# Performance work log

Hardware: AMD Instinct MI355X
Metric: run time of the kernel (lower is better)

The kernel has to match this reference:

```python
import jax, jax.numpy as jnp
import numpy as np

H = 32        # query heads
KV = 8        # key/value heads
D = 128       # head_dim
GROUPS = H // KV
THETA = 10000.0


def _rope_cos_sin(position_ids):
    # position_ids: [B, S] int
    inv_freq = 1.0 / (THETA ** (jnp.arange(0, D, 2, dtype=jnp.float32) / D))  # [D/2]
    freqs = position_ids.astype(jnp.float32)[:, :, None] * inv_freq[None, None, :]  # [B,S,D/2]
    emb = jnp.concatenate([freqs, freqs], axis=-1)  # [B,S,D]
    return jnp.cos(emb), jnp.sin(emb)


def _rotate_half(x):
    x1, x2 = jnp.split(x, 2, axis=-1)
    return jnp.concatenate([-x2, x1], axis=-1)


def _apply_rope(x, cos, sin):
    # x: [B,h,S,D]; cos/sin: [B,S,D] -> broadcast over heads
    return x * cos[:, None, :, :] + _rotate_half(x) * sin[:, None, :, :]


def setup_inputs() -> dict:
    key = jax.random.key(0)
    ks = jax.random.split(key, 8)
    B, S, Dm = 2, 2048, 4096
    scale = lambda d: 1.0 / np.sqrt(d)
    hidden_states = jax.random.normal(ks[0], (B, S, Dm), dtype=jnp.float32)
    position_ids = jnp.broadcast_to(jnp.arange(S, dtype=jnp.int32)[None, :], (B, S))
    Wq = jax.random.normal(ks[1], (Dm, H * D), dtype=jnp.float32) * scale(Dm)
    Wk = jax.random.normal(ks[2], (Dm, KV * D), dtype=jnp.float32) * scale(Dm)
    Wv = jax.random.normal(ks[3], (Dm, KV * D), dtype=jnp.float32) * scale(Dm)
    Wo = jax.random.normal(ks[4], (H * D, Dm), dtype=jnp.float32) * scale(H * D)
    # per-head shift-encoder correction weights (small init so it's a correction)
    Ws_q = jax.random.normal(ks[5], (H, D, D), dtype=jnp.float32) * (0.02 * scale(D))
    Ws_k = jax.random.normal(ks[6], (H, D, D), dtype=jnp.float32) * (0.02 * scale(D))
    return {"hidden_states": hidden_states, "position_ids": position_ids,
            "Wq": Wq, "Wk": Wk, "Wv": Wv, "Wo": Wo, "Ws_q": Ws_q, "Ws_k": Ws_k}


def reference(hidden_states, position_ids, Wq, Wk, Wv, Wo, Ws_q, Ws_k):
    B, S, Dm = hidden_states.shape
    # projections -> [B, heads, S, D]
    q = (hidden_states @ Wq).reshape(B, S, H, D).transpose(0, 2, 1, 3)
    k = (hidden_states @ Wk).reshape(B, S, KV, D).transpose(0, 2, 1, 3)
    v = (hidden_states @ Wv).reshape(B, S, KV, D).transpose(0, 2, 1, 3)
    # RoPE
    cos, sin = _rope_cos_sin(position_ids)
    q = _apply_rope(q, cos, sin)
    k = _apply_rope(k, cos, sin)
    # GQA repeat_kv: [B,KV,S,D] -> [B,H,S,D]
    k = jnp.repeat(k, GROUPS, axis=1)
    v = jnp.repeat(v, GROUPS, axis=1)
    # causal SDPA
    scores = jnp.einsum('bhqd,bhkd->bhqk', q, k) / jnp.sqrt(jnp.float32(D))
    causal = jnp.tril(jnp.ones((S, S), dtype=bool))
    scores = jnp.where(causal[None, None, :, :], scores, jnp.float32(-1e30))
    probs = jax.nn.softmax(scores, axis=-1)
    attn = jnp.einsum('bhqk,bhkd->bhqd', probs, v)  # [B,H,S,D]
    attn = attn.transpose(0, 2, 1, 3)               # [B,S,H,D]
    # shift_encoder.do_shift: per-head linear correction from rotated Q and K
    delta = jnp.einsum('bhsd,hde->bshe', q, Ws_q) + jnp.einsum('bhsd,hde->bshe', k, Ws_k)
    attn = attn + delta
    # output projection
    out = attn.reshape(B, S, H * D) @ Wo
    return out
```

## Files before the change

### kernel.cpp

```cpp
#include <hip/hip_runtime.h>
#include <cstdint>

#define DEV __device__ __forceinline__

typedef __attribute__((ext_vector_type(4))) float  f32x4;
typedef __attribute__((ext_vector_type(8))) short  s16x8;
typedef __attribute__((ext_vector_type(4))) unsigned short u16x4;
typedef __attribute__((ext_vector_type(8))) unsigned short u16x8;

constexpr int B_   = 2;
constexpr int S_   = 2048;
constexpr int DM   = 4096;
constexpr int HQ   = 32;
constexpr int KVH  = 8;
constexpr int DH   = 128;
constexpr int NQKV = 6144;

DEV unsigned short f2bf(float f) {
  union { float f; unsigned u; } c; c.f = f;
  unsigned u = c.u + 0x7FFFu + ((c.u >> 16) & 1u);
  return (unsigned short)(u >> 16);
}
DEV float bf2f(unsigned short h) {
  union { unsigned u; float f; } c; c.u = (unsigned)h << 16; return c.f;
}
DEV void gload16(const void* g, const void* l) {
  __builtin_amdgcn_global_load_lds(
      (const __attribute__((address_space(1))) unsigned int*)(uintptr_t)g,
      (__attribute__((address_space(3))) unsigned int*)(unsigned)(uintptr_t)l,
      16, 0, 0);
}
DEV f32x4 mfma16x16(s16x8 a, s16x8 b, f32x4 c) {
  return __builtin_amdgcn_mfma_f32_16x16x32_bf16(a, b, c, 0, 0, 0);
}

__global__ __launch_bounds__(256) void k_tables(const int* __restrict__ pos,
                                                float* __restrict__ ct,
                                                float* __restrict__ st) {
  int i = blockIdx.x * 256 + threadIdx.x;
  if (i >= B_ * S_ * 64) return;
  int f = i & 63, bs = i >> 6;
  float p   = (float)pos[bs];
  float inv = __builtin_amdgcn_exp2f(-(float)f * 0.20762050593048355f);
  float a   = p * inv;
  ct[i] = cosf(a);
  st[i] = sinf(a);
}

__global__ __launch_bounds__(256) void k_cvt(const float* __restrict__ in,
                                             unsigned short* __restrict__ out,
                                             int n8) {
  int i = blockIdx.x * 256 + threadIdx.x;
  if (i >= n8) return;
  const f32x4* p = (const f32x4*)in + (size_t)2 * i;
  f32x4 a = p[0], b = p[1];
  u16x8 o;
  o[0] = f2bf(a[0]); o[1] = f2bf(a[1]); o[2] = f2bf(a[2]); o[3] = f2bf(a[3]);
  o[4] = f2bf(b[0]); o[5] = f2bf(b[1]); o[6] = f2bf(b[2]); o[7] = f2bf(b[3]);
  ((u16x8*)out)[i] = o;
}

__global__ __launch_bounds__(256) void k_tconv(const float* __restrict__ in,
                                               unsigned short* __restrict__ out,
                                               int R, int C,
                                               unsigned long long ibs,
                                               unsigned long long obs) {
  __shared__ float t[64][65];
  const int r0 = blockIdx.y * 64, c0 = blockIdx.x * 64;
  const float* ib = in + (size_t)blockIdx.z * ibs;
  unsigned short* ob = out + (size_t)blockIdx.z * obs;
  const int tid = threadIdx.x, tr = tid >> 4, c4 = (tid & 15) * 4;
#pragma unroll
  for (int it = 0; it < 4; ++it) {
    int rr = it * 16 + tr;
    f32x4 v = *(const f32x4*)&ib[(size_t)(r0 + rr) * C + (c0 + c4)];
    t[rr][c4 + 0] = v[0]; t[rr][c4 + 1] = v[1];
    t[rr][c4 + 2] = v[2]; t[rr][c4 + 3] = v[3];
  }
  __syncthreads();
#pragma unroll
  for (int it = 0; it < 4; ++it) {
    int cc = it * 16 + tr;
    u16x4 o;
    o[0] = f2bf(t[c4 + 0][cc]); o[1] = f2bf(t[c4 + 1][cc]);
    o[2] = f2bf(t[c4 + 2][cc]); o[3] = f2bf(t[c4 + 3][cc]);
    *(u16x4*)&ob[(size_t)(c0 + cc) * R + (r0 + c4)] = o;
  }
}

template <int BF16OUT>
__global__ __launch_bounds__(512, 2) void k_gemm256(const unsigned short* __restrict__ A,
                                                    const unsigned short* __restrict__ BT,
                                                    void* __restrict__ Cv,
                                                    int M, int N, int K, int NBX) {
  extern __shared__ __align__(16) char L[];
  const int tid = threadIdx.x;
  const int lane = tid & 63, w = tid >> 6;
  const int g = lane >> 4, ml = lane & 15;
  const int wr = w & 1, wc = w >> 1;

  const int cpx = (int)gridDim.x >> 3;
  const int swz = ((int)blockIdx.x & 7) * cpx + ((int)blockIdx.x >> 3);
  const int by = swz / NBX, bx = swz - by * NBX;
  const int bm = by * 256, bn = bx * 256;

  const int srow_l = tid >> 3;
  const int scol_e = (((tid & 7) ^ ((tid >> 3) & 7)) << 3);
  const int nk = K >> 6;

#define STAGE(kt, hf) do {                                                        \
    if ((kt) < nk) {                                                              \
      const unsigned short* sb; char* db;                                         \
      if ((hf) < 2) { sb = A  + (size_t)(bm + (hf) * 128) * K;                    \
                      db = L + ((kt) & 1) * 32768 + (hf) * 16384; }               \
      else          { sb = BT + (size_t)(bn + ((hf) - 2) * 128) * K;              \
                      db = L + 65536 + ((kt) & 1) * 32768 + ((hf) - 2) * 16384; } \
      sb += (size_t)(kt) * 64 + scol_e;                                           \
      _Pragma("unroll")                                                           \
      for (int r_ = 0; r_ < 2; ++r_)                                              \
        gload16(sb + (size_t)(r_ * 64 + srow_l) * K, db + r_ * 8192 + w * 1024);  \
    } } while (0)

  f32x4 Z = {0.f, 0.f, 0.f, 0.f};
  f32x4 acc[8][4];
#pragma unroll
  for (int i = 0; i < 8; ++i)
#pragma unroll
    for (int j = 0; j < 4; ++j) acc[i][j] = Z;
  s16x8 bfr[4][2], afr[2][2];

#define FRAG(base, row, ks)                                                       \
  ((const s16x8*)((base) + ((((row) >> 7) * 16384 + ((row) & 127) * 128 +         \
                             ((ks) * 32 + 8 * g) * 2) ^ (((row) & 7) << 4))))

#define PHASE(q, kbuf, SKT, SHF, VM) do {                                         \
    if ((q) == 0) {                                                               \
      _Pragma("unroll")                                                           \
      for (int nf = 0; nf < 4; ++nf)                                              \
        _Pragma("unroll")                                                         \
        for (int ks = 0; ks < 2; ++ks)                                            \
          bfr[nf][ks] = *FRAG(L + 65536 + (kbuf) * 32768,                         \
                              wc * 64 + nf * 16 + ml, ks);                        \
    }                                                                             \
    _Pragma("unroll")                                                             \
    for (int mm = 0; mm < 2; ++mm)                                                \
      _Pragma("unroll")                                                           \
      for (int ks = 0; ks < 2; ++ks)                                              \
        afr[mm][ks] = *FRAG(L + (kbuf) * 32768,                                   \
                            32 * (2 * (q) + mm) + 16 * wr + ml, ks);              \
    STAGE(SKT, SHF);                                                              \
    if ((VM) == 1) { asm volatile("s_waitcnt vmcnt(6)" ::: "memory"); }           \
    else if ((VM) == 2) {                                                         \
      if (last) { asm volatile("s_waitcnt vmcnt(0)" ::: "memory"); }              \
      else      { asm volatile("s_waitcnt vmcnt(6)" ::: "memory"); }              \
    } else if ((VM) == 3) {                                                       \
      if (!last) { asm volatile("s_waitcnt vmcnt(6)" ::: "memory"); }             \
    }                                                                             \
    __builtin_amdgcn_s_barrier();                                                 \
    asm volatile("s_waitcnt lgkmcnt(0)" ::: "memory");                            \
    __builtin_amdgcn_sched_barrier(0);                                            \
    __builtin_amdgcn_s_setprio(1);                                                \
    _Pragma("unroll")                                                             \
    for (int mm = 0; mm < 2; ++mm)                                                \
      _Pragma("unroll")                                                           \
      for (int nf = 0; nf < 4; ++nf)                                              \
        _Pragma("unroll")                                                         \
        for (int ks = 0; ks < 2; ++ks)                                            \
          acc[2 * (q) + mm][nf] =                                                 \
              mfma16x16(afr[mm][ks], bfr[nf][ks], acc[2 * (q) + mm][nf]);         \
    __builtin_amdgcn_s_setprio(0);                                                \
    __builtin_amdgcn_s_barrier();                                                 \
  } while (0)

  STAGE(0, 0); STAGE(0, 1); STAGE(0, 2); STAGE(0, 3);
  STAGE(1, 2); STAGE(1, 3); STAGE(1, 0);
  asm volatile("s_waitcnt vmcnt(6)" ::: "memory");
  __builtin_amdgcn_s_barrier();

  const int iters = nk >> 1;
  for (int i = 0; i < iters; ++i) {
    const int k0 = 2 * i;
    const bool last = (i == iters - 1);
    PHASE(0, 0, k0 + 1, 1, 0);
    PHASE(1, 0, k0 + 2, 2, 0);
    PHASE(2, 0, k0 + 2, 0, 0);
    PHASE(3, 0, k0 + 2, 3, 2);
    PHASE(0, 1, k0 + 2, 1, 0);
    PHASE(1, 1, k0 + 3, 2, 0);
    PHASE(2, 1, k0 + 3, 3, 0);
    PHASE(3, 1, k0 + 3, 0, 3);
  }
#undef PHASE
#undef FRAG
#undef STAGE

  const int row0 = bm + 16 * wr + 4 * g, col0 = bn + wc * 64 + ml;
#pragma unroll
  for (int m = 0; m < 8; ++m)
#pragma unroll
    for (int nf = 0; nf < 4; ++nf)
#pragma unroll
      for (int r = 0; r < 4; ++r) {
        int row = row0 + 32 * m + r;
        int col = col0 + nf * 16;
        if (BF16OUT)
          ((unsigned short*)Cv)[(size_t)row * N + col] = f2bf(acc[m][nf][r]);
        else
          ((float*)Cv)[(size_t)row * N + col] = acc[m][nf][r];
      }
}

__global__ __launch_bounds__(256) void k_rope(const unsigned short* __restrict__ qkv,
                                              const float* __restrict__ ct,
                                              const float* __restrict__ st,
                                              unsigned short* __restrict__ qr,
                                              unsigned short* __restrict__ kr) {
  const int bs = blockIdx.x;
  const int b = bs >> 11, s = bs & 2047;
  const int tid = threadIdx.x;
  const float* cr = ct + (size_t)bs * 64;
  const float* sr = st + (size_t)bs * 64;
  const unsigned short* row = qkv + (size_t)bs * NQKV;
  {
    int h = tid >> 3, d0 = (tid & 7) * 16;
    u16x8 xs  = *(const u16x8*)&row[h * 128 + d0];
    u16x8 xs2 = *(const u16x8*)&row[h * 128 + d0 + 8];
    u16x8 xp  = *(const u16x8*)&row[h * 128 + (d0 ^ 64)];
    u16x8 xp2 = *(const u16x8*)&row[h * 128 + (d0 ^ 64) + 8];
    float sg = (d0 < 64) ? -1.f : 1.f;
    int ci = d0 & 63;
    u16x8 o1, o2;
#pragma unroll
    for (int j = 0; j < 8; ++j)
      o1[j] = f2bf(bf2f(xs[j]) * cr[ci + j] + sg * bf2f(xp[j]) * sr[ci + j]);
#pragma unroll
    for (int j = 0; j < 8; ++j)
      o2[j] = f2bf(bf2f(xs2[j]) * cr[ci + 8 + j] + sg * bf2f(xp2[j]) * sr[ci + 8 + j]);
    unsigned short* dst = qr + ((size_t)(b * HQ + h) * S_ + s) * DH + d0;
    *(u16x8*)dst = o1;
    *(u16x8*)(dst + 8) = o2;
  }
  if (tid < 64) {
    int kv = tid >> 3, d0 = (tid & 7) * 16;
    const unsigned short* krow = row + HQ * DH + kv * 128;
    u16x8 xs  = *(const u16x8*)&krow[d0];
    u16x8 xs2 = *(const u16x8*)&krow[d0 + 8];
    u16x8 xp  = *(const u16x8*)&krow[d0 ^ 64];
    u16x8 xp2 = *(const u16x8*)&krow[(d0 ^ 64) + 8];
    float sg = (d0 < 64) ? -1.f : 1.f;
    int ci = d0 & 63;
    u16x8 o1, o2;
#pragma unroll
    for (int j = 0; j < 8; ++j)
      o1[j] = f2bf(bf2f(xs[j]) * cr[ci + j] + sg * bf2f(xp[j]) * sr[ci + j]);
#pragma unroll
    for (int j = 0; j < 8; ++j)
      o2[j] = f2bf(bf2f(xs2[j]) * cr[ci + 8 + j] + sg * bf2f(xp2[j]) * sr[ci + 8 + j]);
    unsigned short* dst = kr + ((size_t)(b * KVH + kv) * S_ + s) * DH + d0;
    *(u16x8*)dst = o1;
    *(u16x8*)(dst + 8) = o2;
  }
}

__global__ __launch_bounds__(256) void k_vtrans(const unsigned short* __restrict__ qkv,
                                                unsigned short* __restrict__ vt) {
  __shared__ unsigned short t[64][65];
  const int z = blockIdx.z, b = z >> 3, kv = z & 7;
  const int s0 = blockIdx.x * 64, d0 = blockIdx.y * 64;
  const int tid = threadIdx.x, tr = tid >> 4, c4 = (tid & 15) * 4;
  const unsigned short* src = qkv + (size_t)(b * S_) * NQKV + HQ * DH + KVH * DH + kv * 128;
#pragma unroll
  for (int it = 0; it < 4; ++it) {
    int s = it * 16 + tr;
    u16x4 v = *(const u16x4*)&src[(size_t)(s0 + s) * NQKV + d0 + c4];
    t[s][c4 + 0] = v[0]; t[s][c4 + 1] = v[1];
    t[s][c4 + 2] = v[2]; t[s][c4 + 3] = v[3];
  }
  __syncthreads();
  unsigned short* dst = vt + (size_t)(b * KVH + kv) * DH * S_;
#pragma unroll
  for (int it = 0; it < 4; ++it) {
    int d = it * 16 + tr;
    u16x4 o;
    o[0] = t[c4 + 0][d]; o[1] = t[c4 + 1][d];
    o[2] = t[c4 + 2][d]; o[3] = t[c4 + 3][d];
    *(u16x4*)&dst[(size_t)(d0 + d) * S_ + s0 + c4] = o;
  }
}

__global__ __launch_bounds__(256) void k_attn(const unsigned short* __restrict__ qr,
                                              const unsigned short* __restrict__ kr,
                                              const unsigned short* __restrict__ vt,
                                              unsigned short* __restrict__ att) {
  const int h = blockIdx.y, b = blockIdx.z, kvh = h >> 2;
  const int tid = threadIdx.x, lane = tid & 63, w = tid >> 6;
  const int g = lane >> 4, ml = lane & 15;

  __shared__ unsigned short kvbuf[16384];
  __shared__ unsigned short pbuf[4][32 * 72];
  unsigned short* kl = kvbuf;
  unsigned short* vl = kvbuf + 8192;

  const unsigned short* Kg = kr + (size_t)(b * KVH + kvh) * S_ * DH;
  const unsigned short* Vg = vt + (size_t)(b * KVH + kvh) * DH * S_;
  const float CS = 0.12751745f;
  f32x4 Z = {0.f, 0.f, 0.f, 0.f};

  for (int half = 0; half < 2; ++half) {
    const int qbx = half ? (15 - (int)blockIdx.x) : (int)blockIdx.x;
    const int qb0 = qbx * 128;
    const unsigned short* Qg = qr + ((size_t)(b * HQ + h) * S_ + qb0) * DH;

    __syncthreads();
#pragma unroll
    for (int it = 0; it < 8; ++it) {
      int c = w + 4 * it;
      int off = c * 1024 + lane * 16;
      int row = off >> 8;
      int sch = ((off >> 4) & 15) ^ (row & 7);
      gload16(Qg + (size_t)row * DH + sch * 8, (const char*)kvbuf + c * 1024);
    }
    __syncthreads();
    s16x8 qfr[2][4];
#pragma unroll
    for (int qf = 0; qf < 2; ++qf)
#pragma unroll
      for (int ds = 0; ds < 4; ++ds) {
        int row = 32 * w + 16 * qf + ml;
        int sch = (4 * ds + g) ^ (row & 7);
        qfr[qf][ds] = *(const s16x8*)((const char*)kvbuf + row * 256 + sch * 16);
      }

    float mstate[2] = {-3e30f, -3e30f};
    float lstate[2] = {0.f, 0.f};
    f32x4 oacc[2][8];
#pragma unroll
    for (int i = 0; i < 2; ++i)
#pragma unroll
      for (int j = 0; j < 8; ++j) oacc[i][j] = Z;

    const int ntiles = (qb0 >> 6) + 2;

    for (int t = 0; t < ntiles; ++t) {
      const int kv0 = t * 64;
      __syncthreads();
#pragma unroll
      for (int it = 0; it < 4; ++it) {
        int c = w + 4 * it;
        int off = c * 1024 + lane * 16;
        int row = off >> 8;
        int sch = ((off >> 4) & 15) ^ (row & 7);
        gload16(Kg + (size_t)(kv0 + row) * DH + sch * 8, (const char*)kl + c * 1024);
      }
#pragma unroll
      for (int it = 0; it < 4; ++it) {
        int c = w + 4 * it;
        int off = c * 1024 + lane * 16;
        int row = off >> 7;
        int sch = ((off >> 4) & 7) ^ (row & 7);
        gload16(Vg + (size_t)row * S_ + kv0 + sch * 8, (const char*)vl + c * 1024);
      }
      __syncthreads();

      f32x4 sacc[4][2];
#pragma unroll
      for (int i = 0; i < 4; ++i) { sacc[i][0] = Z; sacc[i][1] = Z; }
#pragma unroll
      for (int ds = 0; ds < 4; ++ds) {
        s16x8 af[4];
#pragma unroll
        for (int kf = 0; kf < 4; ++kf) {
          int row = 16 * kf + ml;
          int sch = (4 * ds + g) ^ (row & 7);
          af[kf] = *(const s16x8*)((const char*)kl + row * 256 + sch * 16);
        }
#pragma unroll
        for (int kf = 0; kf < 4; ++kf)
#pragma unroll
          for (int qf = 0; qf < 2; ++qf)
            sacc[kf][qf] = mfma16x16(af[kf], qfr[qf][ds], sacc[kf][qf]);
      }

      const int qg = qb0 + 32 * w + ml;
      const bool fullTile = (kv0 + 63 <= qb0 + 32 * w);
      float alpha[2];
#pragma unroll
      for (int qf = 0; qf < 2; ++qf) {
        int qq = qg + 16 * qf;
        float mx = -3e30f;
        if (fullTile) {
#pragma unroll
          for (int kf = 0; kf < 4; ++kf)
#pragma unroll
            for (int r = 0; r < 4; ++r) {
              float sv = sacc[kf][qf][r] * CS;
              sacc[kf][qf][r] = sv;
              mx = fmaxf(mx, sv);
            }
        } else {
#pragma unroll
          for (int kf = 0; kf < 4; ++kf)
#pragma unroll
            for (int r = 0; r < 4; ++r) {
              float sv = sacc[kf][qf][r] * CS;
              int kk = kv0 + 16 * kf + 4 * g + r;
              sv = (kk <= qq) ? sv : -3e30f;
              sacc[kf][qf][r] = sv;
              mx = fmaxf(mx, sv);
            }
        }
        mx = fmaxf(mx, __shfl_xor(mx, 16));
        mx = fmaxf(mx, __shfl_xor(mx, 32));
        float mn = fmaxf(mstate[qf], mx);
        alpha[qf] = __builtin_amdgcn_exp2f(mstate[qf] - mn);
        mstate[qf] = mn;
        float ls = 0.f;
#pragma unroll
        for (int kf = 0; kf < 4; ++kf) {
          u16x4 pk;
#pragma unroll
          for (int r = 0; r < 4; ++r) {
            float p = __builtin_amdgcn_exp2f(sacc[kf][qf][r] - mn);
            ls += p;
            pk[r] = f2bf(p);
          }
          *(u16x4*)&pbuf[w][(16 * qf + ml) * 72 + 16 * kf + 4 * g] = pk;
        }
        ls += __shfl_xor(ls, 16);
        ls += __shfl_xor(ls, 32);
        lstate[qf] = lstate[qf] * alpha[qf] + ls;
      }
#pragma unroll
      for (int mf = 0; mf < 2; ++mf)
#pragma unroll
        for (int r = 0; r < 4; ++r) {
          float a = __shfl(alpha[mf], (lane & 48) | (4 * g + r));
#pragma unroll
          for (int nf = 0; nf < 8; ++nf) oacc[mf][nf][r] *= a;
        }
#pragma unroll
      for (int ks = 0; ks < 2; ++ks) {
        s16x8 pa[2];
#pragma unroll
        for (int mf = 0; mf < 2; ++mf)
          pa[mf] = *(const s16x8*)&pbuf[w][(16 * mf + ml) * 72 + 32 * ks + 8 * g];
#pragma unroll
        for (int nf = 0; nf < 8; ++nf) {
          int row = 16 * nf + ml;
          int sch = (4 * ks + g) ^ (row & 7);
          s16x8 bv = *(const s16x8*)((const char*)vl + row * 128 + sch * 16);
#pragma unroll
          for (int mf = 0; mf < 2; ++mf)
            oacc[mf][nf] = mfma16x16(pa[mf], bv, oacc[mf][nf]);
        }
      }
    }

#pragma unroll
    for (int mf = 0; mf < 2; ++mf)
#pragma unroll
      for (int r = 0; r < 4; ++r) {
        float li = __shfl(lstate[mf], (lane & 48) | (4 * g + r));
        float inv = 1.0f / li;
        int rowg = b * S_ + qb0 + 32 * w + 16 * mf + 4 * g + r;
        size_t base = (size_t)rowg * (HQ * DH) + h * DH;
#pragma unroll
        for (int nf = 0; nf < 8; ++nf)
          att[base + 16 * nf + ml] = f2bf(oacc[mf][nf][r] * inv);
      }
  }
}

__global__ __launch_bounds__(256) void k_delta(const unsigned short* __restrict__ qr,
                                               const unsigned short* __restrict__ kr,
                                               const unsigned short* __restrict__ wsq,
                                               const unsigned short* __restrict__ wsk,
                                               unsigned short* __restrict__ att) {
  const int s0 = blockIdx.x * 128, h = blockIdx.y, b = blockIdx.z;
  const int tid = threadIdx.x, lane = tid & 63, w = tid >> 6;
  const int wr = w >> 1, wc = w & 1;
  const int g = lane >> 4, ml = lane & 15;
  __shared__ unsigned short la[128 * 32], lb[128 * 32];
  f32x4 Z = {0.f, 0.f, 0.f, 0.f};
  f32x4 acc[4][4];
#pragma unroll
  for (int i = 0; i < 4; ++i)
#pragma unroll
    for (int j = 0; j < 4; ++j) acc[i][j] = Z;
  const unsigned short* Ab[2] = {
      qr + ((size_t)(b * HQ + h) * S_ + s0) * DH,
      kr + ((size_t)(b * KVH + (h >> 2)) * S_ + s0) * DH};
  const unsigned short* Bb[2] = {wsq + (size_t)h * DH * DH, wsk + (size_t)h * DH * DH};
  for (int pass = 0; pass < 2; ++pass) {
    for (int kt = 0; kt < 4; ++kt) {
      __syncthreads();
#pragma unroll
      for (int it = 0; it < 2; ++it) {
        int c = w + 4 * it;
        int row = c * 16 + (lane >> 2);
        int co = kt * 32 + (lane & 3) * 8;
        gload16(Ab[pass] + (size_t)row * DH + co, (const char*)la + c * 1024);
        gload16(Bb[pass] + (size_t)row * DH + co, (const char*)lb + c * 1024);
      }
      __syncthreads();
      s16x8 af[4], bf[4];
#pragma unroll
      for (int mf = 0; mf < 4; ++mf)
        af[mf] = *(const s16x8*)&la[(wr * 64 + 16 * mf + ml) * 32 + 8 * g];
#pragma unroll
      for (int nf = 0; nf < 4; ++nf)
        bf[nf] = *(const s16x8*)&lb[(wc * 64 + 16 * nf + ml) * 32 + 8 * g];
#pragma unroll
      for (int mf = 0; mf < 4; ++mf)
#pragma unroll
        for (int nf = 0; nf < 4; ++nf)
          acc[mf][nf] = mfma16x16(af[mf], bf[nf], acc[mf][nf]);
    }
  }
#pragma unroll
  for (int mf = 0; mf < 4; ++mf)
#pragma unroll
    for (int nf = 0; nf < 4; ++nf)
#pragma unroll
      for (int r = 0; r < 4; ++r) {
        int row = s0 + wr * 64 + 16 * mf + 4 * g + r;
        size_t idx = ((size_t)(b * S_ + row)) * (HQ * DH) + h * DH + wc * 64 + 16 * nf + ml;
        att[idx] = f2bf(bf2f(att[idx]) + acc[mf][nf][r]);
      }
}

extern "C" void kernel_launch(void* const* d_in, const int* in_sizes, int n_in,
                              void* d_out, int out_size, void* d_ws, size_t ws_size,
                              hipStream_t stream) {
  const float* hidden = (const float*)d_in[0];
  const int*   pos    = (const int*)d_in[1];
  const float* Wq     = (const float*)d_in[2];
  const float* Wk     = (const float*)d_in[3];
  const float* Wv     = (const float*)d_in[4];
  const float* Wo     = (const float*)d_in[5];
  const float* Wsq    = (const float*)d_in[6];
  const float* Wsk    = (const float*)d_in[7];

  char* ws = (char*)d_ws;
  unsigned short* XB    = (unsigned short*)(ws + 0);
  unsigned short* WQKVT = (unsigned short*)(ws + 33554432);
  unsigned short* WOT   = (unsigned short*)(ws + 83886080);
  unsigned short* WSQT  = (unsigned short*)(ws + 117440512);
  unsigned short* WSKT  = (unsigned short*)(ws + 118489088);
  float*          CT    = (float*)(ws + 119537664);
  float*          ST    = (float*)(ws + 120586240);
  unsigned short* QKV   = (unsigned short*)(ws + 121634816);
  unsigned short* QR    = (unsigned short*)(ws + 171966464);
  unsigned short* KR    = (unsigned short*)(ws + 205520896);
  unsigned short* VT    = (unsigned short*)(ws + 213909504);
  unsigned short* ATT   = (unsigned short*)(ws + 222298112);

  k_tables<<<1024, 256, 0, stream>>>(pos, CT, ST);
  k_cvt<<<8192, 256, 0, stream>>>(hidden, XB, 2097152);
  k_tconv<<<dim3(64, 64, 1), 256, 0, stream>>>(Wq, WQKVT, 4096, 4096, 0, 0);
  k_tconv<<<dim3(16, 64, 1), 256, 0, stream>>>(Wk, WQKVT + (size_t)4096 * 4096, 4096, 1024, 0, 0);
  k_tconv<<<dim3(16, 64, 1), 256, 0, stream>>>(Wv, WQKVT + (size_t)5120 * 4096, 4096, 1024, 0, 0);
  k_tconv<<<dim3(64, 64, 1), 256, 0, stream>>>(Wo, WOT, 4096, 4096, 0, 0);
  k_tconv<<<dim3(2, 2, 32), 256, 0, stream>>>(Wsq, WSQT, 128, 128, 16384, 16384);
  k_tconv<<<dim3(2, 2, 32), 256, 0, stream>>>(Wsk, WSKT, 128, 128, 16384, 16384);
  k_gemm256<1><<<dim3(384), 512, 131072, stream>>>(XB, WQKVT, QKV, 4096, 6144, 4096, 24);
  k_rope<<<4096, 256, 0, stream>>>(QKV, CT, ST, QR, KR);
  k_vtrans<<<dim3(32, 2, 16), 256, 0, stream>>>(QKV, VT);
  k_attn<<<dim3(8, 32, 2), 256, 0, stream>>>(QR, KR, VT, ATT);
  k_delta<<<dim3(16, 32, 2), 256, 0, stream>>>(QR, KR, WSQT, WSKT, ATT);
  k_gemm256<0><<<dim3(256), 512, 131072, stream>>>(ATT, WOT, d_out, 4096, 4096, 4096, 16);
}
```

Before: 635.0 us.

## Use 256x128 GEMM tiles and fuse shift-encoder delta into attention

Shrinks the GEMM block tile from 256x256 to 256x128, which doubles the grid and cuts LDS to 96KB, and restructures the staging and phase schedule to match. It also folds the per-head shift-encoder correction into the attention epilogue. The epilogue reuses the Q fragments and the diagonal-block K fragments already in registers, so the separate k_delta kernel and its read-modify-write of ATT go away. The aim is better load balance across CUs and less memory traffic. The costs are lower per-block arithmetic intensity in the GEMM and extra register pressure and LDS loads of the Ws weights inside attention.

```diff
diff --git a/kernel.cpp b/kernel.cpp
--- a/kernel.cpp
+++ b/kernel.cpp
@@ -89,10 +89,10 @@
 }
 
 template <int BF16OUT>
-__global__ __launch_bounds__(512, 2) void k_gemm256(const unsigned short* __restrict__ A,
-                                                    const unsigned short* __restrict__ BT,
-                                                    void* __restrict__ Cv,
-                                                    int M, int N, int K, int NBX) {
+__global__ __launch_bounds__(512, 2) void k_gemmN128(const unsigned short* __restrict__ A,
+                                                     const unsigned short* __restrict__ BT,
+                                                     void* __restrict__ Cv,
+                                                     int M, int N, int K, int NBX) {
   extern __shared__ __align__(16) char L[];
   const int tid = threadIdx.x;
   const int lane = tid & 63, w = tid >> 6;
@@ -102,7 +102,7 @@
   const int cpx = (int)gridDim.x >> 3;
   const int swz = ((int)blockIdx.x & 7) * cpx + ((int)blockIdx.x >> 3);
   const int by = swz / NBX, bx = swz - by * NBX;
-  const int bm = by * 256, bn = bx * 256;
+  const int bm = by * 256, bn = bx * 128;
 
   const int srow_l = tid >> 3;
   const int scol_e = (((tid & 7) ^ ((tid >> 3) & 7)) << 3);
@@ -111,10 +111,10 @@
 #define STAGE(kt, hf) do {                                                        \
     if ((kt) < nk) {                                                              \
       const unsigned short* sb; char* db;                                         \
-      if ((hf) < 2) { sb = A  + (size_t)(bm + (hf) * 128) * K;                    \
-                      db = L + ((kt) & 1) * 32768 + (hf) * 16384; }               \
-      else          { sb = BT + (size_t)(bn + ((hf) - 2) * 128) * K;              \
-                      db = L + 65536 + ((kt) & 1) * 32768 + ((hf) - 2) * 16384; } \
+      if ((hf) < 2) { sb = A + (size_t)(bm + (hf) * 128) * K;                     \
+                      db = L + ((kt) & 1) * 49152 + (hf) * 16384; }               \
+      else          { sb = BT + (size_t)bn * K;                                   \
+                      db = L + ((kt) & 1) * 49152 + 32768; }                      \
       sb += (size_t)(kt) * 64 + scol_e;                                           \
       _Pragma("unroll")                                                           \
       for (int r_ = 0; r_ < 2; ++r_)                                              \
@@ -122,38 +122,40 @@
     } } while (0)
 
   f32x4 Z = {0.f, 0.f, 0.f, 0.f};
-  f32x4 acc[8][4];
-#pragma unroll
-  for (int i = 0; i < 8; ++i)
-#pragma unroll
-    for (int j = 0; j < 4; ++j) acc[i][j] = Z;
-  s16x8 bfr[4][2], afr[2][2];
+  f32x4 acc[8][2];
+#pragma unroll
+  for (int i = 0; i < 8; ++i) { acc[i][0] = Z; acc[i][1] = Z; }
+  s16x8 afr[4][2], bfr[2][2];
 
 #define FRAG(base, row, ks)                                                       \
   ((const s16x8*)((base) + ((((row) >> 7) * 16384 + ((row) & 127) * 128 +         \
                              ((ks) * 32 + 8 * g) * 2) ^ (((row) & 7) << 4))))
 
-#define PHASE(q, kbuf, SKT, SHF, VM) do {                                         \
+#define PHASE(q, kbuf, SK1, H1, SK2, H2, VM) do {                                 \
     if ((q) == 0) {                                                               \
       _Pragma("unroll")                                                           \
-      for (int nf = 0; nf < 4; ++nf)                                              \
+      for (int nf = 0; nf < 2; ++nf)                                              \
         _Pragma("unroll")                                                         \
         for (int ks = 0; ks < 2; ++ks)                                            \
-          bfr[nf][ks] = *FRAG(L + 65536 + (kbuf) * 32768,                         \
-                              wc * 64 + nf * 16 + ml, ks);                        \
+          bfr[nf][ks] = *FRAG(L + (kbuf) * 49152 + 32768,                         \
+                              wc * 32 + nf * 16 + ml, ks);                        \
     }                                                                             \
     _Pragma("unroll")                                                             \
-    for (int mm = 0; mm < 2; ++mm)                                                \
+    for (int mm = 0; mm < 4; ++mm)                                                \
       _Pragma("unroll")                                                           \
       for (int ks = 0; ks < 2; ++ks)                                              \
-        afr[mm][ks] = *FRAG(L + (kbuf) * 32768,                                   \
-                            32 * (2 * (q) + mm) + 16 * wr + ml, ks);              \
-    STAGE(SKT, SHF);                                                              \
-    if ((VM) == 1) { asm volatile("s_waitcnt vmcnt(6)" ::: "memory"); }           \
-    else if ((VM) == 2) {                                                         \
+        afr[mm][ks] = *FRAG(L + (kbuf) * 49152,                                   \
+                            32 * (4 * (q) + mm) + 16 * wr + ml, ks);              \
+    STAGE(SK1, H1);                                                               \
+    if ((H2) >= 0) STAGE(SK2, H2);                                                \
+    if ((VM) == 0) { asm volatile("s_waitcnt vmcnt(6)" ::: "memory"); }           \
+    else if ((VM) == 1) {                                                         \
+      if (last) { asm volatile("s_waitcnt vmcnt(2)" ::: "memory"); }              \
+      else      { asm volatile("s_waitcnt vmcnt(6)" ::: "memory"); }              \
+    } else if ((VM) == 2) {                                                       \
       if (last) { asm volatile("s_waitcnt vmcnt(0)" ::: "memory"); }              \
       else      { asm volatile("s_waitcnt vmcnt(6)" ::: "memory"); }              \
-    } else if ((VM) == 3) {                                                       \
+    } else {                                                                      \
       if (!last) { asm volatile("s_waitcnt vmcnt(6)" ::: "memory"); }             \
     }                                                                             \
     __builtin_amdgcn_s_barrier();                                                 \
@@ -161,44 +163,40 @@
     __builtin_amdgcn_sched_barrier(0);                                            \
     __builtin_amdgcn_s_setprio(1);                                                \
     _Pragma("unroll")                                                             \
-    for (int mm = 0; mm < 2; ++mm)                                                \
+    for (int mm = 0; mm < 4; ++mm)                                                \
       _Pragma("unroll")                                                           \
-      for (int nf = 0; nf < 4; ++nf)                                              \
+      for (int nf = 0; nf < 2; ++nf)                                              \
         _Pragma("unroll")                                                         \
         for (int ks = 0; ks < 2; ++ks)                                            \
-          acc[2 * (q) + mm][nf] =                                                 \
-              mfma16x16(afr[mm][ks], bfr[nf][ks], acc[2 * (q) + mm][nf]);         \
+          acc[4 * (q) + mm][nf] =                                                 \
+              mfma16x16(afr[mm][ks], bfr[nf][ks], acc[4 * (q) + mm][nf]);         \
     __builtin_amdgcn_s_setprio(0);                                                \
     __builtin_amdgcn_s_barrier();                                                 \
   } while (0)
 
-  STAGE(0, 0); STAGE(0, 1); STAGE(0, 2); STAGE(0, 3);
-  STAGE(1, 2); STAGE(1, 3); STAGE(1, 0);
-  asm volatile("s_waitcnt vmcnt(6)" ::: "memory");
+  STAGE(0, 0); STAGE(0, 1); STAGE(0, 2);
+  STAGE(1, 0); STAGE(1, 2);
+  asm volatile("s_waitcnt vmcnt(4)" ::: "memory");
   __builtin_amdgcn_s_barrier();
 
   const int iters = nk >> 1;
   for (int i = 0; i < iters; ++i) {
-    const int k0 = 2 * i;
+    const int t = 2 * i;
     const bool last = (i == iters - 1);
-    PHASE(0, 0, k0 + 1, 1, 0);
-    PHASE(1, 0, k0 + 2, 2, 0);
-    PHASE(2, 0, k0 + 2, 0, 0);
-    PHASE(3, 0, k0 + 2, 3, 2);
-    PHASE(0, 1, k0 + 2, 1, 0);
-    PHASE(1, 1, k0 + 3, 2, 0);
-    PHASE(2, 1, k0 + 3, 3, 0);
-    PHASE(3, 1, k0 + 3, 0, 3);
+    PHASE(0, 0, t + 1, 1, -1, -1, 0);
+    PHASE(1, 0, t + 2, 0, t + 2, 2, 1);
+    PHASE(0, 1, t + 2, 1, -1, -1, 2);
+    PHASE(1, 1, t + 3, 0, t + 3, 2, 3);
   }
 #undef PHASE
 #undef FRAG
 #undef STAGE
 
-  const int row0 = bm + 16 * wr + 4 * g, col0 = bn + wc * 64 + ml;
+  const int row0 = bm + 16 * wr + 4 * g, col0 = bn + wc * 32 + ml;
 #pragma unroll
   for (int m = 0; m < 8; ++m)
 #pragma unroll
-    for (int nf = 0; nf < 4; ++nf)
+    for (int nf = 0; nf < 2; ++nf)
 #pragma unroll
       for (int r = 0; r < 4; ++r) {
         int row = row0 + 32 * m + r;
@@ -291,6 +289,8 @@
 __global__ __launch_bounds__(256) void k_attn(const unsigned short* __restrict__ qr,
                                               const unsigned short* __restrict__ kr,
                                               const unsigned short* __restrict__ vt,
+                                              const unsigned short* __restrict__ wsq,
+                                              const unsigned short* __restrict__ wsk,
                                               unsigned short* __restrict__ att) {
   const int h = blockIdx.y, b = blockIdx.z, kvh = h >> 2;
   const int tid = threadIdx.x, lane = tid & 63, w = tid >> 6;
@@ -334,6 +334,7 @@
     float mstate[2] = {-3e30f, -3e30f};
     float lstate[2] = {0.f, 0.f};
     f32x4 oacc[2][8];
+    s16x8 kfr[2][4];
 #pragma unroll
     for (int i = 0; i < 2; ++i)
 #pragma unroll
@@ -379,6 +380,20 @@
 #pragma unroll
           for (int qf = 0; qf < 2; ++qf)
             sacc[kf][qf] = mfma16x16(af[kf], qfr[qf][ds], sacc[kf][qf]);
+      }
+
+      {
+        int rel = kv0 - qb0;
+        if (rel == ((w >> 1) << 6)) {
+#pragma unroll
+          for (int qf = 0; qf < 2; ++qf)
+#pragma unroll
+            for (int ds = 0; ds < 4; ++ds) {
+              int row = 32 * w + 16 * qf + ml - rel;
+              int sch = (4 * ds + g) ^ (row & 7);
+              kfr[qf][ds] = *(const s16x8*)((const char*)kl + row * 256 + sch * 16);
+            }
+        }
       }
 
       const int qg = qb0 + 32 * w + ml;
@@ -462,71 +477,53 @@
       for (int r = 0; r < 4; ++r) {
         float li = __shfl(lstate[mf], (lane & 48) | (4 * g + r));
         float inv = 1.0f / li;
+#pragma unroll
+        for (int nf = 0; nf < 8; ++nf) oacc[mf][nf][r] *= inv;
+      }
+
+#pragma unroll
+    for (int pass = 0; pass < 2; ++pass) {
+      const unsigned short* Wg =
+          (pass == 0 ? wsq : wsk) + (size_t)h * DH * DH;
+      __syncthreads();
+#pragma unroll
+      for (int it = 0; it < 8; ++it) {
+        int c = w + 4 * it;
+        int off = c * 1024 + lane * 16;
+        int row = off >> 8;
+        int sch = ((off >> 4) & 15) ^ (row & 7);
+        gload16(Wg + (size_t)row * DH + sch * 8, (const char*)kvbuf + c * 1024);
+      }
+      __syncthreads();
+#pragma unroll
+      for (int nf = 0; nf < 8; ++nf) {
+        s16x8 wf[4];
+#pragma unroll
+        for (int ds = 0; ds < 4; ++ds) {
+          int row = 16 * nf + ml;
+          int sch = (4 * ds + g) ^ (row & 7);
+          wf[ds] = *(const s16x8*)((const char*)kvbuf + row * 256 + sch * 16);
+        }
+#pragma unroll
+        for (int qf = 0; qf < 2; ++qf)
+#pragma unroll
+          for (int ds = 0; ds < 4; ++ds)
+            oacc[qf][nf] = mfma16x16(pass == 0 ? qfr[qf][ds] : kfr[qf][ds],
+                                     wf[ds], oacc[qf][nf]);
+      }
+    }
+
+#pragma unroll
+    for (int mf = 0; mf < 2; ++mf)
+#pragma unroll
+      for (int r = 0; r < 4; ++r) {
         int rowg = b * S_ + qb0 + 32 * w + 16 * mf + 4 * g + r;
         size_t base = (size_t)rowg * (HQ * DH) + h * DH;
 #pragma unroll
         for (int nf = 0; nf < 8; ++nf)
-          att[base + 16 * nf + ml] = f2bf(oacc[mf][nf][r] * inv);
-      }
-  }
-}
-
-__global__ __launch_bounds__(256) void k_delta(const unsigned short* __restrict__ qr,
-                                               const unsigned short* __restrict__ kr,
-                                               const unsigned short* __restrict__ wsq,
-                                               const unsigned short* __restrict__ wsk,
-                                               unsigned short* __restrict__ att) {
-  const int s0 = blockIdx.x * 128, h = blockIdx.y, b = blockIdx.z;
-  const int tid = threadIdx.x, lane = tid & 63, w = tid >> 6;
-  const int wr = w >> 1, wc = w & 1;
-  const int g = lane >> 4, ml = lane & 15;
-  __shared__ unsigned short la[128 * 32], lb[128 * 32];
-  f32x4 Z = {0.f, 0.f, 0.f, 0.f};
-  f32x4 acc[4][4];
-#pragma unroll
-  for (int i = 0; i < 4; ++i)
-#pragma unroll
-    for (int j = 0; j < 4; ++j) acc[i][j] = Z;
-  const unsigned short* Ab[2] = {
-      qr + ((size_t)(b * HQ + h) * S_ + s0) * DH,
-      kr + ((size_t)(b * KVH + (h >> 2)) * S_ + s0) * DH};
-  const unsigned short* Bb[2] = {wsq + (size_t)h * DH * DH, wsk + (size_t)h * DH * DH};
-  for (int pass = 0; pass < 2; ++pass) {
-    for (int kt = 0; kt < 4; ++kt) {
-      __syncthreads();
-#pragma unroll
-      for (int it = 0; it < 2; ++it) {
-        int c = w + 4 * it;
-        int row = c * 16 + (lane >> 2);
-        int co = kt * 32 + (lane & 3) * 8;
-        gload16(Ab[pass] + (size_t)row * DH + co, (const char*)la + c * 1024);
-        gload16(Bb[pass] + (size_t)row * DH + co, (const char*)lb + c * 1024);
-      }
-      __syncthreads();
-      s16x8 af[4], bf[4];
-#pragma unroll
-      for (int mf = 0; mf < 4; ++mf)
-        af[mf] = *(const s16x8*)&la[(wr * 64 + 16 * mf + ml) * 32 + 8 * g];
-#pragma unroll
-      for (int nf = 0; nf < 4; ++nf)
-        bf[nf] = *(const s16x8*)&lb[(wc * 64 + 16 * nf + ml) * 32 + 8 * g];
-#pragma unroll
-      for (int mf = 0; mf < 4; ++mf)
-#pragma unroll
-        for (int nf = 0; nf < 4; ++nf)
-          acc[mf][nf] = mfma16x16(af[mf], bf[nf], acc[mf][nf]);
-    }
-  }
-#pragma unroll
-  for (int mf = 0; mf < 4; ++mf)
-#pragma unroll
-    for (int nf = 0; nf < 4; ++nf)
-#pragma unroll
-      for (int r = 0; r < 4; ++r) {
-        int row = s0 + wr * 64 + 16 * mf + 4 * g + r;
-        size_t idx = ((size_t)(b * S_ + row)) * (HQ * DH) + h * DH + wc * 64 + 16 * nf + ml;
-        att[idx] = f2bf(bf2f(att[idx]) + acc[mf][nf][r]);
-      }
+          att[base + 16 * nf + ml] = f2bf(oacc[mf][nf][r]);
+      }
+  }
 }
 
 extern "C" void kernel_launch(void* const* d_in, const int* in_sizes, int n_in,
@@ -563,10 +560,9 @@
   k_tconv<<<dim3(64, 64, 1), 256, 0, stream>>>(Wo, WOT, 4096, 4096, 0, 0);
   k_tconv<<<dim3(2, 2, 32), 256, 0, stream>>>(Wsq, WSQT, 128, 128, 16384, 16384);
   k_tconv<<<dim3(2, 2, 32), 256, 0, stream>>>(Wsk, WSKT, 128, 128, 16384, 16384);
-  k_gemm256<1><<<dim3(384), 512, 131072, stream>>>(XB, WQKVT, QKV, 4096, 6144, 4096, 24);
+  k_gemmN128<1><<<dim3(768), 512, 98304, stream>>>(XB, WQKVT, QKV, 4096, 6144, 4096, 48);
   k_rope<<<4096, 256, 0, stream>>>(QKV, CT, ST, QR, KR);
   k_vtrans<<<dim3(32, 2, 16), 256, 0, stream>>>(QKV, VT);
-  k_attn<<<dim3(8, 32, 2), 256, 0, stream>>>(QR, KR, VT, ATT);
-  k_delta<<<dim3(16, 32, 2), 256, 0, stream>>>(QR, KR, WSQT, WSKT, ATT);
-  k_gemm256<0><<<dim3(256), 512, 131072, stream>>>(ATT, WOT, d_out, 4096, 4096, 4096, 16);
-}
+  k_attn<<<dim3(8, 32, 2), 256, 0, stream>>>(QR, KR, VT, WSQT, WSKT, ATT);
+  k_gemmN128<0><<<dim3(512), 512, 98304, stream>>>(ATT, WOT, d_out, 4096, 4096, 4096, 32);
+}
```

Result: no change. 647.5 us (+2.0%).
